# Kernel optimization log

Hardware: AMD Instinct MI355X
Metric: run time of the kernel (lower is better)

The kernel has to match this reference:

```python
import jax, jax.numpy as jnp
import numpy as np

NEG_SLOPE = 0.2

def gat_conv(x, W, a_src, a_dst, b, src, dst, n_nodes):
    # x: [N, F_in], W: [F_in, F_out], a_src/a_dst: [F_out], b: [F_out]
    h = x @ W                                   # [N, F_out]
    alpha_s = h @ a_src                         # [N]
    alpha_d = h @ a_dst                         # [N]
    e = jax.nn.leaky_relu(alpha_s[src] + alpha_d[dst], NEG_SLOPE)  # [E]
    # scatter-softmax over incoming edges of each dst node
    m = jax.ops.segment_max(e, dst, num_segments=n_nodes)
    m = jnp.where(jnp.isfinite(m), m, 0.0)      # nodes with no in-edges
    p = jnp.exp(e - m[dst])
    denom = jax.ops.segment_sum(p, dst, num_segments=n_nodes)
    alpha = p / (denom[dst] + 1e-16)            # [E]
    out = jax.ops.segment_sum(alpha[:, None] * h[src], dst, num_segments=n_nodes)
    return out + b

def setup_inputs() -> dict:
    key = jax.random.key(0)
    N, E, F_IN, H, C = 100000, 1600000, 128, 64, 2
    ks = jax.random.split(key, 10)
    x = jax.random.normal(ks[0], (N, F_IN), dtype=jnp.float32)
    edge_index = jax.random.randint(ks[1], (2, E), 0, N, dtype=jnp.int64)
    s1 = 1.0 / np.sqrt(F_IN)
    s2 = 1.0 / np.sqrt(H)
    return {
        "x": x,
        "edge_index": edge_index,
        "W1": jax.random.normal(ks[2], (F_IN, H), dtype=jnp.float32) * s1,
        "a_src1": jax.random.normal(ks[3], (H,), dtype=jnp.float32) * s2,
        "a_dst1": jax.random.normal(ks[4], (H,), dtype=jnp.float32) * s2,
        "b1": jnp.zeros((H,), dtype=jnp.float32),
        "W2": jax.random.normal(ks[5], (H, C), dtype=jnp.float32) * s2,
        "a_src2": jax.random.normal(ks[6], (C,), dtype=jnp.float32),
        "a_dst2": jax.random.normal(ks[7], (C,), dtype=jnp.float32),
        "b2": jnp.zeros((C,), dtype=jnp.float32),
    }

def reference(x, edge_index, W1, a_src1, a_dst1, b1, W2, a_src2, a_dst2, b2):
    N = x.shape[0]
    loops = jnp.arange(N, dtype=edge_index.dtype)   # GATConv add_self_loops=True
    src = jnp.concatenate([edge_index[0], loops])
    dst = jnp.concatenate([edge_index[1], loops])
    h = gat_conv(x, W1, a_src1, a_dst1, b1, src, dst, N)
    h = jax.nn.relu(h)
    # F.dropout with training=False is identity (eval mode)
    out = gat_conv(h, W2, a_src2, a_dst2, b2, src, dst, N)
    return out
```

## Files before the change

kernel.cpp:

```cpp
#include <hip/hip_runtime.h>
#include <math.h>

constexpr int N_NODES = 100000;
constexpr int N_EDGES = 1600000;
constexpr int F_IN    = 128;
constexpr int F_H     = 64;
constexpr float NEG_SLOPE = 0.2f;

constexpr int NBUCK  = (N_NODES + 255) / 256;
constexpr int BUFCAP = 6144;
constexpr int LCAP   = 6144;
constexpr int CPAD   = 16;

constexpr int SB   = 256;
constexpr int EPT  = 4;
constexpr int EPR  = 256 * EPT;
constexpr int G    = 16;
constexpr int BCAP = 48;

__device__ inline float lrelu(float v) { return v > 0.f ? v : NEG_SLOPE * v; }
__device__ inline float blo(unsigned u) { return __uint_as_float(u << 16); }
__device__ inline float bhi(unsigned u) { return __uint_as_float(u & 0xFFFF0000u); }
__device__ inline unsigned bf16hi(float f) {
    unsigned u = __float_as_uint(f);
    return (u + 0x7FFFu + ((u >> 16) & 1u)) & 0xFFFF0000u;
}
__device__ inline unsigned bf16lo(float f) {
    unsigned u = __float_as_uint(f);
    return (u + 0x7FFFu + ((u >> 16) & 1u)) >> 16;
}

__global__ __launch_bounds__(256) void k_gemm1(
    const float* __restrict__ x, const float* __restrict__ W1,
    const float* __restrict__ a_s, const float* __restrict__ a_d,
    unsigned* __restrict__ h1b, float* __restrict__ as1, float* __restrict__ ad1)
{
    __shared__ float vsP[4][64];
    __shared__ float vdP[4][64];

    const int lane = threadIdx.x & 63;
    const int w    = __builtin_amdgcn_readfirstlane(threadIdx.x >> 6);
    const int fo   = w * 16;
    const int row  = blockIdx.x * 64 + lane;
    const bool valid = row < N_NODES;

    float acc[16];
#pragma unroll
    for (int i = 0; i < 16; ++i) acc[i] = 0.f;

    if (valid) {
        const float4* __restrict__ xr = (const float4*)(x + (size_t)row * F_IN);
        float4 xv = xr[0];
        for (int k4 = 0; k4 < F_IN / 4; ++k4) {
            const float4 xn = xr[(k4 + 1) & (F_IN / 4 - 1)];
            const float* __restrict__ wk = W1 + (size_t)k4 * 4 * F_H + fo;
#pragma unroll
            for (int kk = 0; kk < 4; ++kk) {
                const float xs = (kk == 0) ? xv.x : (kk == 1) ? xv.y : (kk == 2) ? xv.z : xv.w;
                const float* __restrict__ ws = wk + kk * F_H;
#pragma unroll
                for (int i = 0; i < 16; ++i)
                    acc[i] = fmaf(xs, ws[i], acc[i]);
            }
            xv = xn;
        }
    }

    float vs = 0.f, vd = 0.f;
#pragma unroll
    for (int i = 0; i < 16; ++i) {
        vs = fmaf(acc[i], a_s[fo + i], vs);
        vd = fmaf(acc[i], a_d[fo + i], vd);
    }
    vsP[w][lane] = vs;
    vdP[w][lane] = vd;
    __syncthreads();
    if (w == 0 && valid) {
        as1[row] = vsP[0][lane] + vsP[1][lane] + vsP[2][lane] + vsP[3][lane];
        ad1[row] = vdP[0][lane] + vdP[1][lane] + vdP[2][lane] + vdP[3][lane];
    }

    if (valid) {
        unsigned up[8];
#pragma unroll
        for (int i = 0; i < 8; ++i)
            up[i] = bf16lo(acc[2 * i]) | bf16hi(acc[2 * i + 1]);
        uint4* __restrict__ hr = (uint4*)(h1b + (size_t)row * 32 + w * 8);
        hr[0] = make_uint4(up[0], up[1], up[2], up[3]);
        hr[1] = make_uint4(up[4], up[5], up[6], up[7]);
    }
}

__global__ __launch_bounds__(256) void k_bucketize_staged(
    const int* __restrict__ ei, int* __restrict__ gcur, unsigned* __restrict__ buf)
{
    __shared__ unsigned bin_buf[NBUCK][BCAP];
    __shared__ int bin_cnt[NBUCK];

    const int t = threadIdx.x;
    for (int i = t; i < NBUCK; i += 256) bin_cnt[i] = 0;
    __syncthreads();

    const int per = N_EDGES / SB;
    const int e0 = blockIdx.x * per;
    const int e1 = (blockIdx.x == SB - 1) ? N_EDGES : (e0 + per);

    int cs[EPT], cd[EPT];
#pragma unroll
    for (int q = 0; q < EPT; ++q) {
        const int i = e0 + q * 256 + t;
        cs[q] = (i < e1) ? ei[i] : -1;
        cd[q] = (i < e1) ? ei[N_EDGES + i] : 0;
    }

    for (int base = e0; base < e1; base += EPR) {
        int ls[EPT], ld[EPT];
#pragma unroll
        for (int q = 0; q < EPT; ++q) { ls[q] = cs[q]; ld[q] = cd[q]; }
        const int nbase = base + EPR;
        if (nbase < e1) {
#pragma unroll
            for (int q = 0; q < EPT; ++q) {
                const int i = nbase + q * 256 + t;
                cs[q] = (i < e1) ? ei[i] : -1;
                cd[q] = (i < e1) ? ei[N_EDGES + i] : 0;
            }
        }
#pragma unroll
        for (int q = 0; q < EPT; ++q) {
            if (ls[q] >= 0) {
                const int b = ld[q] >> 8;
                const int pos = atomicAdd(&bin_cnt[b], 1);
                if (pos < BCAP)
                    bin_buf[b][pos] = ((unsigned)ls[q] << 8) | (unsigned)(ld[q] & 255);
            }
        }
        __syncthreads();
        for (int bb = t; bb < NBUCK; bb += 256) {
            const int cnt = bin_cnt[bb];
            if (cnt >= G) {
                const int take = cnt & ~(G - 1);
                const int gbase = atomicAdd(&gcur[bb * CPAD], take);
                if (gbase + take <= BUFCAP) {
                    unsigned* __restrict__ dst = buf + (size_t)bb * BUFCAP + gbase;
                    const int src0 = cnt - take;
                    for (int u = 0; u < take; u += 4) {
                        uint4 v;
                        v.x = bin_buf[bb][src0 + u];
                        v.y = bin_buf[bb][src0 + u + 1];
                        v.z = bin_buf[bb][src0 + u + 2];
                        v.w = bin_buf[bb][src0 + u + 3];
                        *(uint4*)(dst + u) = v;
                    }
                }
                bin_cnt[bb] = cnt - take;
            }
        }
        __syncthreads();
    }
    for (int bb = t; bb < NBUCK; bb += 256) {
        const int cnt = bin_cnt[bb];
        if (cnt > 0) {
            const int gbase = atomicAdd(&gcur[bb * CPAD], cnt);
            if (gbase + cnt <= BUFCAP) {
                unsigned* __restrict__ dst = buf + (size_t)bb * BUFCAP + gbase;
                for (int u = 0; u < cnt; ++u) dst[u] = bin_buf[bb][u];
            }
        }
    }
}

__global__ __launch_bounds__(512) void k_bscan(const int* __restrict__ gcur, int* __restrict__ boff)
{
    __shared__ int sm[512];
    const int t = threadIdx.x;
    const int m = (t < NBUCK) ? min(gcur[t * CPAD], BUFCAP) : 0;
    sm[t] = m;
    __syncthreads();
    for (int o = 1; o < 512; o <<= 1) {
        int a = (t >= o) ? sm[t - o] : 0;
        __syncthreads();
        sm[t] += a;
        __syncthreads();
    }
    if (t < NBUCK) boff[t] = sm[t] - m;
}

__global__ __launch_bounds__(1024) void k_csr_build(
    const int* __restrict__ gcur, const unsigned* __restrict__ buf, const int* __restrict__ boff,
    int* __restrict__ row_start, int* __restrict__ csr)
{
    __shared__ int lcsr[LCAP];
    __shared__ int hist[256];
    __shared__ int lstart[257];
    __shared__ int lcur[256];

    const int b  = blockIdx.x;
    const int t  = threadIdx.x;
    const int nd = min(256, N_NODES - (b << 8));
    const int m  = min(gcur[b * CPAD], BUFCAP);
    const unsigned* __restrict__ sb = buf + (size_t)b * BUFCAP;

    if (t < 256) hist[t] = 0;
    __syncthreads();

    for (int i = t; i < m; i += 1024) atomicAdd(&hist[sb[i] & 255], 1);
    __syncthreads();

    for (int o = 1; o < 256; o <<= 1) {
        int a = 0;
        if (t < 256 && t >= o) a = hist[t - o];
        __syncthreads();
        if (t < 256) hist[t] += a;
        __syncthreads();
    }
    if (t < 256) { lstart[t + 1] = hist[t]; lcur[t] = 0; }
    if (t == 0) lstart[0] = 0;
    __syncthreads();

    for (int i = t; i < m; i += 1024) {
        const unsigned v = sb[i];
        const int dl = v & 255;
        const int p  = atomicAdd(&lcur[dl], 1);
        const int pp = lstart[dl] + p;
        if (pp < LCAP) lcsr[pp] = (int)(v >> 8);
    }
    __syncthreads();

    const int gb   = boff[b];
    const int mtot = lstart[256];
    for (int i = t; i < mtot; i += 1024) csr[gb + i] = lcsr[i];
    if (t < nd) row_start[(b << 8) + t + 1] = gb + lstart[t + 1];
    if (b == 0 && t == 0) row_start[0] = 0;
}

__global__ __launch_bounds__(256, 4) void k_agg1(
    const int* __restrict__ row_start, const int* __restrict__ csr,
    const float* __restrict__ as1, const float* __restrict__ ad1,
    const unsigned* __restrict__ h1b,
    const float* __restrict__ b1, const float* __restrict__ W2,
    const float* __restrict__ a_s2, const float* __restrict__ a_d2,
    float* __restrict__ h2, float* __restrict__ as2, float* __restrict__ ad2)
{
    const int n = blockIdx.x * 4 + (threadIdx.x >> 6);
    const int j = threadIdx.x & 63;
    if (n >= N_NODES) return;

    const int g  = j >> 3;
    const int oq = (j & 7) << 2;

    const int r0  = row_start[n];
    const int deg = row_start[n + 1] - r0;
    const float ad = ad1[n];

    float acc0[8], acc1[8];
#pragma unroll
    for (int i = 0; i < 8; ++i) { acc0[i] = 0.f; acc1[i] = 0.f; }
    float den_l = 0.f;

#define FMA8(ACC, P, U)                                            \
    ACC[0] = fmaf(P, blo(U.x), ACC[0]); ACC[1] = fmaf(P, bhi(U.x), ACC[1]); \
    ACC[2] = fmaf(P, blo(U.y), ACC[2]); ACC[3] = fmaf(P, bhi(U.y), ACC[3]); \
    ACC[4] = fmaf(P, blo(U.z), ACC[4]); ACC[5] = fmaf(P, bhi(U.z), ACC[5]); \
    ACC[6] = fmaf(P, blo(U.w), ACC[6]); ACC[7] = fmaf(P, bhi(U.w), ACC[7]);
#define LD8(S) (*(const uint4*)(h1b + ((size_t)(S) << 5) + oq))

    if (deg <= 63) {
        int sj = n;
        if (j < deg) sj = csr[r0 + j];
        const float aj = as1[sj];
        const int s0 = __shfl(sj, g,      64);
        const int s1 = __shfl(sj, 8 + g,  64);
        const uint4 u0 = LD8(s0);
        const uint4 u1 = LD8(s1);
        float pj = 0.f;
        if (j <= deg) pj = __expf(lrelu(aj + ad));
        den_l = pj;
        const float p0 = __shfl(pj, g,      64);
        const float p1 = __shfl(pj, 8 + g,  64);

        const int tot = deg + 1;
        const bool t16 = tot > 16, t24 = tot > 24, t32 = tot > 32;
        int s2, s3; uint4 u2, u3; float p2, p3;
        if (t16) { s2 = __shfl(sj, 16 + g, 64); u2 = LD8(s2); p2 = __shfl(pj, 16 + g, 64); }
        if (t24) { s3 = __shfl(sj, 24 + g, 64); u3 = LD8(s3); p3 = __shfl(pj, 24 + g, 64); }
        FMA8(acc0, p0, u0) FMA8(acc1, p1, u1)
        if (t16) { FMA8(acc0, p2, u2) }
        if (t24) { FMA8(acc1, p3, u3) }
        if (t32) {
            for (int base = 32; base < tot; base += 8) {
                const int   sA = __shfl(sj, base + g, 64);
                const float pA = __shfl(pj, base + g, 64);
                const uint4 ua = LD8(sA);
                FMA8(acc0, pA, ua)
            }
        }
    } else {
        {
            const float ps = __expf(lrelu(as1[n] + ad));
            if (j == 0) den_l += ps;
            if (g == 0) {
                const uint4 uv = LD8(n);
                FMA8(acc0, ps, uv)
            }
        }
        for (int cb = r0; cb < r0 + deg; cb += 64) {
            const int cnt = min(64, r0 + deg - cb);
            int sj = 0; float pj = 0.f;
            if (j < cnt) { sj = csr[cb + j]; pj = __expf(lrelu(as1[sj] + ad)); }
            den_l += pj;
            for (int base = 0; base < cnt; base += 16) {
                const int   sA = __shfl(sj, base + g, 64);
                const float pA = __shfl(pj, base + g, 64);
                const uint4 ua = LD8(sA);
                FMA8(acc0, pA, ua)
                if (base + 8 < cnt) {
                    const int   sB = __shfl(sj, base + 8 + g, 64);
                    const float pB = __shfl(pj, base + 8 + g, 64);
                    const uint4 ub = LD8(sB);
                    FMA8(acc1, pB, ub)
                }
            }
        }
    }
#undef FMA8
#undef LD8

    float den = den_l;
#pragma unroll
    for (int o = 32; o; o >>= 1) den += __shfl_xor(den, o, 64);

#pragma unroll
    for (int i = 0; i < 8; ++i) acc0[i] += acc1[i];
#pragma unroll
    for (int o = 8; o <= 32; o <<= 1) {
#pragma unroll
        for (int i = 0; i < 8; ++i) acc0[i] += __shfl_xor(acc0[i], o, 64);
    }

    const float inv = 1.f / (den + 1e-16f);
    const int ob = (j & 7) << 3;
    const float4 b0 = *(const float4*)(b1 + ob);
    const float4 b4 = *(const float4*)(b1 + ob + 4);
    float v[8];
    v[0] = acc0[0] * inv + b0.x; v[1] = acc0[1] * inv + b0.y;
    v[2] = acc0[2] * inv + b0.z; v[3] = acc0[3] * inv + b0.w;
    v[4] = acc0[4] * inv + b4.x; v[5] = acc0[5] * inv + b4.y;
    v[6] = acc0[6] * inv + b4.z; v[7] = acc0[7] * inv + b4.w;
#pragma unroll
    for (int i = 0; i < 8; ++i) v[i] = v[i] > 0.f ? v[i] : 0.f;

    const float4* __restrict__ wq = (const float4*)(W2 + 2 * ob);
    const float4 w0 = wq[0], w1 = wq[1], w2 = wq[2], w3 = wq[3];
    float c0 = v[0] * w0.x + v[1] * w0.z + v[2] * w1.x + v[3] * w1.z
             + v[4] * w2.x + v[5] * w2.z + v[6] * w3.x + v[7] * w3.z;
    float c1 = v[0] * w0.y + v[1] * w0.w + v[2] * w1.y + v[3] * w1.w
             + v[4] * w2.y + v[5] * w2.w + v[6] * w3.y + v[7] * w3.w;
#pragma unroll
    for (int o = 1; o <= 4; o <<= 1) {
        c0 += __shfl_xor(c0, o, 64);
        c1 += __shfl_xor(c1, o, 64);
    }
    if (j == 0) {
        h2[n * 2 + 0] = c0;
        h2[n * 2 + 1] = c1;
        as2[n] = c0 * a_s2[0] + c1 * a_s2[1];
        ad2[n] = c0 * a_d2[0] + c1 * a_d2[1];
    }
}

__global__ __launch_bounds__(256) void k_agg2_wave(
    const int* __restrict__ row_start, const int* __restrict__ csr,
    const float* __restrict__ as2, const float* __restrict__ ad2,
    const float* __restrict__ h2, const float* __restrict__ b2,
    float* __restrict__ out)
{
    const int n = blockIdx.x * 4 + (threadIdx.x >> 6);
    const int j = threadIdx.x & 63;
    if (n >= N_NODES) return;
    const int r0  = row_start[n];
    const int deg = row_start[n + 1] - r0;
    const float ad = ad2[n];
    const float2* __restrict__ h22 = (const float2*)h2;

    float den_l = 0.f, x0 = 0.f, x1 = 0.f;
    if (deg <= 63) {
        int sj = n;
        if (j < deg) sj = csr[r0 + j];
        const float  aj = as2[sj];
        const float2 hv = h22[sj];
        float p = 0.f;
        if (j <= deg) p = __expf(lrelu(aj + ad));
        den_l = p; x0 = p * hv.x; x1 = p * hv.y;
    } else {
        if (j == 0) {
            const float p = __expf(lrelu(as2[n] + ad));
            const float2 hv = h22[n];
            den_l = p; x0 = p * hv.x; x1 = p * hv.y;
        }
        for (int idx = r0 + j; idx < r0 + deg; idx += 64) {
            const int s = csr[idx];
            const float p = __expf(lrelu(as2[s] + ad));
            const float2 hv = h22[s];
            den_l += p; x0 = fmaf(p, hv.x, x0); x1 = fmaf(p, hv.y, x1);
        }
    }
#pragma unroll
    for (int o = 32; o; o >>= 1) {
        den_l += __shfl_xor(den_l, o, 64);
        x0    += __shfl_xor(x0, o, 64);
        x1    += __shfl_xor(x1, o, 64);
    }
    if (j == 0) {
        const float inv = 1.f / (den_l + 1e-16f);
        out[n * 2 + 0] = x0 * inv + b2[0];
        out[n * 2 + 1] = x1 * inv + b2[1];
    }
}

extern "C" void kernel_launch(void* const* d_in, const int* in_sizes, int n_in,
                              void* d_out, int out_size, void* d_ws, size_t ws_size,
                              hipStream_t stream)
{
    const float* x    = (const float*)d_in[0];
    const int*   ei   = (const int*)d_in[1];
    const float* W1   = (const float*)d_in[2];
    const float* as1w = (const float*)d_in[3];
    const float* ad1w = (const float*)d_in[4];
    const float* b1   = (const float*)d_in[5];
    const float* W2   = (const float*)d_in[6];
    const float* as2w = (const float*)d_in[7];
    const float* ad2w = (const float*)d_in[8];
    const float* b2   = (const float*)d_in[9];
    float* out = (float*)d_out;

    float* ws = (float*)d_ws;
    size_t off = 0;
    unsigned* h1b = (unsigned*)(ws + off); off += (size_t)N_NODES * 32;
    float* as1 = ws + off; off += N_NODES;
    float* ad1 = ws + off; off += N_NODES;
    float* h2  = ws + off; off += (size_t)N_NODES * 2;
    float* as2 = ws + off; off += N_NODES;
    float* ad2 = ws + off; off += N_NODES;
    int* gcur      = (int*)(ws + off); off += NBUCK * CPAD;
    unsigned* buf  = (unsigned*)(ws + off); off += (size_t)NBUCK * BUFCAP;
    int* boff      = (int*)(ws + off); off += NBUCK + 1;
    int* row_start = (int*)(ws + off); off += N_NODES + 1;
    int* csr       = (int*)(ws + off); off += N_EDGES;

    hipMemsetAsync(gcur, 0, NBUCK * CPAD * sizeof(int), stream);

    k_gemm1           <<<(N_NODES + 63) / 64, 256, 0, stream>>>(x, W1, as1w, ad1w, h1b, as1, ad1);
    k_bucketize_staged<<<SB, 256, 0, stream>>>(ei, gcur, buf);
    k_bscan           <<<1, 512, 0, stream>>>(gcur, boff);
    k_csr_build       <<<NBUCK, 1024, 0, stream>>>(gcur, buf, boff, row_start, csr);
    k_agg1            <<<(N_NODES + 3) / 4, 256, 0, stream>>>(
        row_start, csr, as1, ad1, h1b, b1, W2, as2w, ad2w, h2, as2, ad2);
    k_agg2_wave       <<<(N_NODES + 3) / 4, 256, 0, stream>>>(row_start, csr, as2, ad2, h2, b2, out);
}
```

Measured before the change: 243.7 us.

## Fuse GEMM1 with edge bucketization and fold bucket scan into CSR build

```diff
diff --git a/kernel.cpp b/kernel.cpp
--- a/kernel.cpp
+++ b/kernel.cpp
@@ -17,6 +17,8 @@
 constexpr int EPR  = 256 * EPT;
 constexpr int G    = 16;
 constexpr int BCAP = 48;
+
+constexpr int GEMM_BLOCKS = (N_NODES + 63) / 64;
 
 __device__ inline float lrelu(float v) { return v > 0.f ? v : NEG_SLOPE * v; }
 __device__ inline float blo(unsigned u) { return __uint_as_float(u << 16); }
@@ -30,18 +32,97 @@
     return (u + 0x7FFFu + ((u >> 16) & 1u)) >> 16;
 }
 
-__global__ __launch_bounds__(256) void k_gemm1(
+__global__ __launch_bounds__(256) void k_gemm1_bucketize(
     const float* __restrict__ x, const float* __restrict__ W1,
     const float* __restrict__ a_s, const float* __restrict__ a_d,
-    unsigned* __restrict__ h1b, float* __restrict__ as1, float* __restrict__ ad1)
+    unsigned* __restrict__ h1b, float* __restrict__ as1, float* __restrict__ ad1,
+    const int* __restrict__ ei, int* __restrict__ gcur, unsigned* __restrict__ buf)
 {
-    __shared__ float vsP[4][64];
-    __shared__ float vdP[4][64];
-
-    const int lane = threadIdx.x & 63;
-    const int w    = __builtin_amdgcn_readfirstlane(threadIdx.x >> 6);
+    __shared__ union SM {
+        struct { unsigned bin_buf[NBUCK][BCAP]; int bin_cnt[NBUCK]; } bk;
+        struct { float vsP[4][64]; float vdP[4][64]; } gm;
+    } sm;
+
+    const int t = threadIdx.x;
+
+    if (blockIdx.x < SB) {
+        for (int i = t; i < NBUCK; i += 256) sm.bk.bin_cnt[i] = 0;
+        __syncthreads();
+
+        const int per = N_EDGES / SB;
+        const int e0 = blockIdx.x * per;
+        const int e1 = (blockIdx.x == SB - 1) ? N_EDGES : (e0 + per);
+
+        int cs[EPT], cd[EPT];
+#pragma unroll
+        for (int q = 0; q < EPT; ++q) {
+            const int i = e0 + q * 256 + t;
+            cs[q] = (i < e1) ? ei[i] : -1;
+            cd[q] = (i < e1) ? ei[N_EDGES + i] : 0;
+        }
+
+        for (int base = e0; base < e1; base += EPR) {
+            int ls[EPT], ld[EPT];
+#pragma unroll
+            for (int q = 0; q < EPT; ++q) { ls[q] = cs[q]; ld[q] = cd[q]; }
+            const int nbase = base + EPR;
+            if (nbase < e1) {
+#pragma unroll
+                for (int q = 0; q < EPT; ++q) {
+                    const int i = nbase + q * 256 + t;
+                    cs[q] = (i < e1) ? ei[i] : -1;
+                    cd[q] = (i < e1) ? ei[N_EDGES + i] : 0;
+                }
+            }
+#pragma unroll
+            for (int q = 0; q < EPT; ++q) {
+                if (ls[q] >= 0) {
+                    const int b = ld[q] >> 8;
+                    const int pos = atomicAdd(&sm.bk.bin_cnt[b], 1);
+                    if (pos < BCAP)
+                        sm.bk.bin_buf[b][pos] = ((unsigned)ls[q] << 8) | (unsigned)(ld[q] & 255);
+                }
+            }
+            __syncthreads();
+            for (int bb = t; bb < NBUCK; bb += 256) {
+                const int cnt = sm.bk.bin_cnt[bb];
+                if (cnt >= G) {
+                    const int take = cnt & ~(G - 1);
+                    const int gbase = atomicAdd(&gcur[bb * CPAD], take);
+                    if (gbase + take <= BUFCAP) {
+                        unsigned* __restrict__ dst = buf + (size_t)bb * BUFCAP + gbase;
+                        const int src0 = cnt - take;
+                        for (int u = 0; u < take; u += 4) {
+                            uint4 v;
+                            v.x = sm.bk.bin_buf[bb][src0 + u];
+                            v.y = sm.bk.bin_buf[bb][src0 + u + 1];
+                            v.z = sm.bk.bin_buf[bb][src0 + u + 2];
+                            v.w = sm.bk.bin_buf[bb][src0 + u + 3];
+                            *(uint4*)(dst + u) = v;
+                        }
+                    }
+                    sm.bk.bin_cnt[bb] = cnt - take;
+                }
+            }
+            __syncthreads();
+        }
+        for (int bb = t; bb < NBUCK; bb += 256) {
+            const int cnt = sm.bk.bin_cnt[bb];
+            if (cnt > 0) {
+                const int gbase = atomicAdd(&gcur[bb * CPAD], cnt);
+                if (gbase + cnt <= BUFCAP) {
+                    unsigned* __restrict__ dst = buf + (size_t)bb * BUFCAP + gbase;
+                    for (int u = 0; u < cnt; ++u) dst[u] = sm.bk.bin_buf[bb][u];
+                }
+            }
+        }
+        return;
+    }
+
+    const int lane = t & 63;
+    const int w    = __builtin_amdgcn_readfirstlane(t >> 6);
     const int fo   = w * 16;
-    const int row  = blockIdx.x * 64 + lane;
+    const int row  = (blockIdx.x - SB) * 64 + lane;
     const bool valid = row < N_NODES;
 
     float acc[16];
@@ -72,12 +153,12 @@
         vs = fmaf(acc[i], a_s[fo + i], vs);
         vd = fmaf(acc[i], a_d[fo + i], vd);
     }
-    vsP[w][lane] = vs;
-    vdP[w][lane] = vd;
+    sm.gm.vsP[w][lane] = vs;
+    sm.gm.vdP[w][lane] = vd;
     __syncthreads();
     if (w == 0 && valid) {
-        as1[row] = vsP[0][lane] + vsP[1][lane] + vsP[2][lane] + vsP[3][lane];
-        ad1[row] = vdP[0][lane] + vdP[1][lane] + vdP[2][lane] + vdP[3][lane];
+        as1[row] = sm.gm.vsP[0][lane] + sm.gm.vsP[1][lane] + sm.gm.vsP[2][lane] + sm.gm.vsP[3][lane];
+        ad1[row] = sm.gm.vdP[0][lane] + sm.gm.vdP[1][lane] + sm.gm.vdP[2][lane] + sm.gm.vdP[3][lane];
     }
 
     if (valid) {
@@ -91,109 +172,16 @@
     }
 }
 
-__global__ __launch_bounds__(256) void k_bucketize_staged(
-    const int* __restrict__ ei, int* __restrict__ gcur, unsigned* __restrict__ buf)
-{
-    __shared__ unsigned bin_buf[NBUCK][BCAP];
-    __shared__ int bin_cnt[NBUCK];
-
-    const int t = threadIdx.x;
-    for (int i = t; i < NBUCK; i += 256) bin_cnt[i] = 0;
-    __syncthreads();
-
-    const int per = N_EDGES / SB;
-    const int e0 = blockIdx.x * per;
-    const int e1 = (blockIdx.x == SB - 1) ? N_EDGES : (e0 + per);
-
-    int cs[EPT], cd[EPT];
-#pragma unroll
-    for (int q = 0; q < EPT; ++q) {
-        const int i = e0 + q * 256 + t;
-        cs[q] = (i < e1) ? ei[i] : -1;
-        cd[q] = (i < e1) ? ei[N_EDGES + i] : 0;
-    }
-
-    for (int base = e0; base < e1; base += EPR) {
-        int ls[EPT], ld[EPT];
-#pragma unroll
-        for (int q = 0; q < EPT; ++q) { ls[q] = cs[q]; ld[q] = cd[q]; }
-        const int nbase = base + EPR;
-        if (nbase < e1) {
-#pragma unroll
-            for (int q = 0; q < EPT; ++q) {
-                const int i = nbase + q * 256 + t;
-                cs[q] = (i < e1) ? ei[i] : -1;
-                cd[q] = (i < e1) ? ei[N_EDGES + i] : 0;
-            }
-        }
-#pragma unroll
-        for (int q = 0; q < EPT; ++q) {
-            if (ls[q] >= 0) {
-                const int b = ld[q] >> 8;
-                const int pos = atomicAdd(&bin_cnt[b], 1);
-                if (pos < BCAP)
-                    bin_buf[b][pos] = ((unsigned)ls[q] << 8) | (unsigned)(ld[q] & 255);
-            }
-        }
-        __syncthreads();
-        for (int bb = t; bb < NBUCK; bb += 256) {
-            const int cnt = bin_cnt[bb];
-            if (cnt >= G) {
-                const int take = cnt & ~(G - 1);
-                const int gbase = atomicAdd(&gcur[bb * CPAD], take);
-                if (gbase + take <= BUFCAP) {
-                    unsigned* __restrict__ dst = buf + (size_t)bb * BUFCAP + gbase;
-                    const int src0 = cnt - take;
-                    for (int u = 0; u < take; u += 4) {
-                        uint4 v;
-                        v.x = bin_buf[bb][src0 + u];
-                        v.y = bin_buf[bb][src0 + u + 1];
-                        v.z = bin_buf[bb][src0 + u + 2];
-                        v.w = bin_buf[bb][src0 + u + 3];
-                        *(uint4*)(dst + u) = v;
-                    }
-                }
-                bin_cnt[bb] = cnt - take;
-            }
-        }
-        __syncthreads();
-    }
-    for (int bb = t; bb < NBUCK; bb += 256) {
-        const int cnt = bin_cnt[bb];
-        if (cnt > 0) {
-            const int gbase = atomicAdd(&gcur[bb * CPAD], cnt);
-            if (gbase + cnt <= BUFCAP) {
-                unsigned* __restrict__ dst = buf + (size_t)bb * BUFCAP + gbase;
-                for (int u = 0; u < cnt; ++u) dst[u] = bin_buf[bb][u];
-            }
-        }
-    }
-}
-
-__global__ __launch_bounds__(512) void k_bscan(const int* __restrict__ gcur, int* __restrict__ boff)
-{
-    __shared__ int sm[512];
-    const int t = threadIdx.x;
-    const int m = (t < NBUCK) ? min(gcur[t * CPAD], BUFCAP) : 0;
-    sm[t] = m;
-    __syncthreads();
-    for (int o = 1; o < 512; o <<= 1) {
-        int a = (t >= o) ? sm[t - o] : 0;
-        __syncthreads();
-        sm[t] += a;
-        __syncthreads();
-    }
-    if (t < NBUCK) boff[t] = sm[t] - m;
-}
-
 __global__ __launch_bounds__(1024) void k_csr_build(
-    const int* __restrict__ gcur, const unsigned* __restrict__ buf, const int* __restrict__ boff,
+    const int* __restrict__ gcur, const unsigned* __restrict__ buf,
     int* __restrict__ row_start, int* __restrict__ csr)
 {
     __shared__ int lcsr[LCAP];
     __shared__ int hist[256];
     __shared__ int lstart[257];
     __shared__ int lcur[256];
+    __shared__ int redsm[16];
+    __shared__ int gb_sm;
 
     const int b  = blockIdx.x;
     const int t  = threadIdx.x;
@@ -201,7 +189,19 @@
     const int m  = min(gcur[b * CPAD], BUFCAP);
     const unsigned* __restrict__ sb = buf + (size_t)b * BUFCAP;
 
+    int part = 0;
+    for (int i = t; i < b; i += 1024) part += min(gcur[i * CPAD], BUFCAP);
+#pragma unroll
+    for (int o = 32; o; o >>= 1) part += __shfl_xor(part, o, 64);
+    if ((t & 63) == 0) redsm[t >> 6] = part;
     if (t < 256) hist[t] = 0;
+    __syncthreads();
+    if (t == 0) {
+        int s = 0;
+#pragma unroll
+        for (int i = 0; i < 16; ++i) s += redsm[i];
+        gb_sm = s;
+    }
     __syncthreads();
 
     for (int i = t; i < m; i += 1024) atomicAdd(&hist[sb[i] & 255], 1);
@@ -227,7 +227,7 @@
     }
     __syncthreads();
 
-    const int gb   = boff[b];
+    const int gb   = gb_sm;
     const int mtot = lstart[256];
     for (int i = t; i < mtot; i += 1024) csr[gb + i] = lcsr[i];
     if (t < nd) row_start[(b << 8) + t + 1] = gb + lstart[t + 1];
@@ -444,16 +444,14 @@
     float* ad2 = ws + off; off += N_NODES;
     int* gcur      = (int*)(ws + off); off += NBUCK * CPAD;
     unsigned* buf  = (unsigned*)(ws + off); off += (size_t)NBUCK * BUFCAP;
-    int* boff      = (int*)(ws + off); off += NBUCK + 1;
     int* row_start = (int*)(ws + off); off += N_NODES + 1;
     int* csr       = (int*)(ws + off); off += N_EDGES;
 
     hipMemsetAsync(gcur, 0, NBUCK * CPAD * sizeof(int), stream);
 
-    k_gemm1           <<<(N_NODES + 63) / 64, 256, 0, stream>>>(x, W1, as1w, ad1w, h1b, as1, ad1);
-    k_bucketize_staged<<<SB, 256, 0, stream>>>(ei, gcur, buf);
-    k_bscan           <<<1, 512, 0, stream>>>(gcur, boff);
-    k_csr_build       <<<NBUCK, 1024, 0, stream>>>(gcur, buf, boff, row_start, csr);
+    k_gemm1_bucketize <<<SB + GEMM_BLOCKS, 256, 0, stream>>>(
+        x, W1, as1w, ad1w, h1b, as1, ad1, ei, gcur, buf);
+    k_csr_build       <<<NBUCK, 1024, 0, stream>>>(gcur, buf, row_start, csr);
     k_agg1            <<<(N_NODES + 3) / 4, 256, 0, stream>>>(
         row_start, csr, as1, ad1, h1b, b1, W2, as2w, ad2w, h2, as2, ad2);
     k_agg2_wave       <<<(N_NODES + 3) / 4, 256, 0, stream>>>(row_start, csr, as2, ad2, h2, b2, out);
```

New measurement: 238.0 us. -2.3%, faster.
